# Performance work log

Measured on AMD Instinct MI355X. Metric: run time of the kernel, lower is better.

Reference implementation:

```python
import jax, jax.numpy as jnp
import numpy as np

B, N, F, U = 4, 4096, 256, 128
NEG = -1.0e9


def setup_inputs() -> dict:
    key = jax.random.key(0)
    k1, k2, k3, k4, k5 = jax.random.split(key, 5)
    inputs = jax.random.normal(k1, (B, N, F), dtype=jnp.float32)
    # Glorot-normal-like scales
    w = jax.random.normal(k2, (F, U), dtype=jnp.float32) * np.sqrt(2.0 / (F + U)).astype(np.float32)
    ai = jax.random.normal(k3, (U, N), dtype=jnp.float32) * np.sqrt(2.0 / (U + N)).astype(np.float32)
    aj = jax.random.normal(k4, (U, N), dtype=jnp.float32) * np.sqrt(2.0 / (U + N)).astype(np.float32)
    a = (jax.random.uniform(k5, (N, N)) < 0.004).astype(jnp.float32)
    adj = jnp.maximum(a, a.T)
    return {"inputs": inputs, "w": w, "ai": ai, "aj": aj, "adj": adj}


def reference(inputs, w, ai, aj, adj):
    # f: [B, N, U]
    f = jnp.einsum('bnf,fu->bnu', inputs, w)
    # self_attn[b,i,j] = (f ai)[b,i,j]; other_attn = transpose([0,2,1]) of (f aj)
    self_attn = jnp.einsum('bnu,um->bnm', f, ai)          # [B, N, N]
    other_attn = jnp.einsum('bnu,um->bmn', f, aj)         # transposed [B, N, N]
    mask = adj + jnp.eye(N, dtype=adj.dtype)              # allow self + neighbors
    attn = self_attn + other_attn + NEG * (1.0 - mask)
    attn = jax.nn.softmax(attn, axis=1)                   # softmax over rows (axis=1)
    # out[b,j,u] = sum_i f[b,i,u] * attn[b,i,j]
    out = jnp.einsum('biu,bij->bju', f, attn)
    return jax.nn.relu(out), attn
```

## Files before the change

kernel.cpp:

```cpp
#include <hip/hip_runtime.h>
#include <hip/hip_bf16.h>

#define NN 4096
#define UU 128
#define BB 4
#define FF 256
#define MAXD 128

__device__ __forceinline__ unsigned short f2bf(float x) {
    unsigned int u = __float_as_uint(x);
    unsigned int r = (u + 0x7fffu + ((u >> 16) & 1u)) >> 16;
    return (unsigned short)r;
}
__device__ __forceinline__ float bf2f(unsigned short h) {
    return __uint_as_float(((unsigned int)h) << 16);
}

template <int CTRL, int RMASK>
__device__ __forceinline__ float dpp_step(float x) {
    int ti = __builtin_amdgcn_update_dpp(0, __float_as_int(x), CTRL, RMASK, 0xf, true);
    return x + __int_as_float(ti);
}
__device__ __forceinline__ float wave_sum_dpp(float x) {
    x = dpp_step<0x111, 0xf>(x);
    x = dpp_step<0x112, 0xf>(x);
    x = dpp_step<0x114, 0xf>(x);
    x = dpp_step<0x118, 0xf>(x);
    x = dpp_step<0x142, 0xa>(x);
    x = dpp_step<0x143, 0xc>(x);
    return __int_as_float(__builtin_amdgcn_readlane(__float_as_int(x), 63));
}

__global__ __launch_bounds__(256) void transpose2(const float* __restrict__ ai,
                                                  const float* __restrict__ aj,
                                                  unsigned short* __restrict__ aiT,
                                                  unsigned short* __restrict__ ajT) {
    __shared__ float tile[32][33];
    const float* src = blockIdx.z ? aj : ai;
    unsigned short* dst = blockIdx.z ? ajT : aiT;
    int n0 = blockIdx.x * 32;
    int u0 = blockIdx.y * 32;
    int tx = threadIdx.x;
    int ty = threadIdx.y;
    for (int r = 0; r < 32; r += 8)
        tile[ty + r][tx] = src[(size_t)(u0 + ty + r) * NN + n0 + tx];
    __syncthreads();
    for (int r = 0; r < 32; r += 8)
        dst[(size_t)(n0 + ty + r) * UU + u0 + tx] = f2bf(tile[tx][ty + r]);
}

__global__ __launch_bounds__(256) void fgemm(const float* __restrict__ A,
                                             const float* __restrict__ Wm,
                                             unsigned short* __restrict__ F) {
    __shared__ float As[64][36];
    __shared__ float Ws[64][132];
    int t = threadIdx.x;
    int r0 = blockIdx.x * 32;
    int cg = t & 31;
    int rg = t >> 5;
    float acc[4][4] = {};

    for (int kc = 0; kc < FF; kc += 64) {
        {
            int row = t >> 3;
            int kb = (t & 7) * 8;
            const float* ap = A + (size_t)(r0 + row) * FF + kc + kb;
            float4 v0 = *(const float4*)(ap);
            float4 v1 = *(const float4*)(ap + 4);
            As[kb + 0][row] = v0.x; As[kb + 1][row] = v0.y;
            As[kb + 2][row] = v0.z; As[kb + 3][row] = v0.w;
            As[kb + 4][row] = v1.x; As[kb + 5][row] = v1.y;
            As[kb + 6][row] = v1.z; As[kb + 7][row] = v1.w;
        }
#pragma unroll
        for (int q = 0; q < 8; q++) {
            int idx = q * 256 + t;
            int k = idx >> 5;
            int c4 = (idx & 31) * 4;
            *(float4*)&Ws[k][c4] = *(const float4*)(Wm + (size_t)(kc + k) * UU + c4);
        }
        __syncthreads();
#pragma unroll 8
        for (int kk = 0; kk < 64; kk++) {
            float4 a4 = *(const float4*)&As[kk][rg * 4];
            float4 w4 = *(const float4*)&Ws[kk][cg * 4];
            acc[0][0] += a4.x * w4.x; acc[0][1] += a4.x * w4.y; acc[0][2] += a4.x * w4.z; acc[0][3] += a4.x * w4.w;
            acc[1][0] += a4.y * w4.x; acc[1][1] += a4.y * w4.y; acc[1][2] += a4.y * w4.z; acc[1][3] += a4.y * w4.w;
            acc[2][0] += a4.z * w4.x; acc[2][1] += a4.z * w4.y; acc[2][2] += a4.z * w4.z; acc[2][3] += a4.z * w4.w;
            acc[3][0] += a4.w * w4.x; acc[3][1] += a4.w * w4.y; acc[3][2] += a4.w * w4.z; acc[3][3] += a4.w * w4.w;
        }
        __syncthreads();
    }
#pragma unroll
    for (int i = 0; i < 4; i++) {
        ushort4 h;
        h.x = f2bf(acc[i][0]); h.y = f2bf(acc[i][1]);
        h.z = f2bf(acc[i][2]); h.w = f2bf(acc[i][3]);
        *(ushort4*)(F + (size_t)(r0 + rg * 4 + i) * UU + cg * 4) = h;
    }
}

__global__ __launch_bounds__(256) void scan_adj(const float* __restrict__ adj,
                                                unsigned short* __restrict__ csc,
                                                int* __restrict__ cnt,
                                                int* __restrict__ dblf) {
    __shared__ unsigned short tmp[MAXD];
    __shared__ int c, d;
    int j = blockIdx.x, tid = threadIdx.x;
    if (tid == 0) { c = 0; d = 0; }
    __syncthreads();
    const float4* row = (const float4*)(adj + (size_t)j * NN);
#pragma unroll
    for (int k = 0; k < 4; k++) {
        int q = tid + k * 256;
        float4 v = row[q];
        int base = q * 4;
        float vals[4] = {v.x, v.y, v.z, v.w};
#pragma unroll
        for (int t = 0; t < 4; t++) {
            int i = base + t;
            bool nz = (vals[t] != 0.0f);
            if (i == j) { if (nz) d = 1; nz = true; }
            if (nz) {
                int p = atomicAdd(&c, 1);
                if (p < MAXD) tmp[p] = (unsigned short)i;
            }
        }
    }
    __syncthreads();
    int M = c < MAXD ? c : MAXD;
    if (tid < M) csc[(size_t)j * MAXD + tid] = tmp[tid];
    if (tid == 0) { cnt[j] = M; dblf[j] = d; }
}

__global__ __launch_bounds__(256) void gat_cols(const unsigned short* __restrict__ csc,
                                                const int* __restrict__ cnt,
                                                const int* __restrict__ dblf,
                                                const unsigned short* __restrict__ f,
                                                const unsigned short* __restrict__ aiT,
                                                const unsigned short* __restrict__ ajT,
                                                float* __restrict__ out,
                                                float* __restrict__ attn) {
    __shared__ unsigned short sidx[MAXD];
    int j = blockIdx.x, tid = threadIdx.x;
    int lane = tid & 63, b = tid >> 6;
    int M = cnt[j];
    int oneh = dblf[j];
    if (tid < MAXD) sidx[tid] = csc[(size_t)j * MAXD + tid];

    const unsigned short* fb = f + (size_t)b * NN * UU;
    ushort2 fjh = *(const ushort2*)(fb + (size_t)j * UU + 2 * lane);
    float fjx = bf2f(fjh.x), fjy = bf2f(fjh.y);

    if (oneh) {
        if (lane == 0) attn[((size_t)(b * NN + j)) * NN + j] = 1.0f;
        float2 o;
        o.x = fjx > 0.0f ? fjx : 0.0f;
        o.y = fjy > 0.0f ? fjy : 0.0f;
        *(float2*)(out + ((size_t)(b * NN + j)) * UU + 2 * lane) = o;
        return;
    }
    __syncthreads();

    ushort2 aih = *(const ushort2*)(aiT + (size_t)j * UU + 2 * lane);
    float aix = bf2f(aih.x), aiy = bf2f(aih.y);
    float denom = 0.0f, acc0 = 0.0f, acc1 = 0.0f;
    float keep0 = 0.0f, keep1 = 0.0f;
    for (int e = 0; e < M; e++) {
        int i = sidx[e];
        ushort2 fih = *(const ushort2*)(fb + (size_t)i * UU + 2 * lane);
        ushort2 ajh = *(const ushort2*)(ajT + (size_t)i * UU + 2 * lane);
        float fix = bf2f(fih.x), fiy = bf2f(fih.y);
        float p = fix * aix + fiy * aiy + fjx * bf2f(ajh.x) + fjy * bf2f(ajh.y);
        float ex = __expf(wave_sum_dpp(p));
        denom += ex;
        acc0 += ex * fix;
        acc1 += ex * fiy;
        if ((e & 63) == lane) { if (e < 64) keep0 = ex; else keep1 = ex; }
    }
    float inv = 1.0f / denom;

    float2 o;
    o.x = acc0 * inv; o.y = acc1 * inv;
    o.x = o.x > 0.0f ? o.x : 0.0f;
    o.y = o.y > 0.0f ? o.y : 0.0f;
    *(float2*)(out + ((size_t)(b * NN + j)) * UU + 2 * lane) = o;

    if (lane < M)
        attn[((size_t)(b * NN + sidx[lane])) * NN + j] = keep0 * inv;
    if (lane + 64 < M)
        attn[((size_t)(b * NN + sidx[lane + 64])) * NN + j] = keep1 * inv;
}

extern "C" void kernel_launch(void* const* d_in, const int* in_sizes, int n_in,
                              void* d_out, int out_size, void* d_ws, size_t ws_size,
                              hipStream_t stream) {
    const float* inputs = (const float*)d_in[0];
    const float* w      = (const float*)d_in[1];
    const float* ai     = (const float*)d_in[2];
    const float* aj     = (const float*)d_in[3];
    const float* adj    = (const float*)d_in[4];

    float* out  = (float*)d_out;
    float* attn = out + (size_t)BB * NN * UU;

    unsigned short* f   = (unsigned short*)d_ws;
    unsigned short* aiT = f + (size_t)BB * NN * UU;
    unsigned short* ajT = aiT + (size_t)NN * UU;
    unsigned short* csc = ajT + (size_t)NN * UU;
    int* cnt  = (int*)(csc + (size_t)NN * MAXD);
    int* dblf = cnt + NN;

    (void)hipMemsetAsync(attn, 0, (size_t)BB * NN * NN * sizeof(float), stream);

    transpose2<<<dim3(NN / 32, UU / 32, 2), dim3(32, 8), 0, stream>>>(ai, aj, aiT, ajT);
    fgemm<<<dim3((BB * NN) / 32), 256, 0, stream>>>(inputs, w, f);
    scan_adj<<<NN, 256, 0, stream>>>(adj, csc, cnt, dblf);
    gat_cols<<<NN, 256, 0, stream>>>(csc, cnt, dblf, f, aiT, ajT, out, attn);
}
```

Measured before the change: 429.2 us.

## Fuse attn zero-fill into GAT kernel and defer sparse scatter to separate pass

Replaces the separate memset of the 256MB attention output with extra blocks in the GAT kernel that zero it using nontemporal vector stores. This lets zeroing overlap with the sparse attention compute. Softmax weights are staged to a workspace buffer, and a new kernel scatters them into attn after zeroing is guaranteed complete. The cost is one extra launch and a small staging buffer, and the gain depends on whether the fused zero blocks run faster than hipMemset.

```diff
diff --git a/kernel.cpp b/kernel.cpp
--- a/kernel.cpp
+++ b/kernel.cpp
@@ -6,6 +6,9 @@
 #define BB 4
 #define FF 256
 #define MAXD 128
+#define ZB 1024
+
+typedef float fv4 __attribute__((ext_vector_type(4)));
 
 __device__ __forceinline__ unsigned short f2bf(float x) {
     unsigned int u = __float_as_uint(x);
@@ -133,27 +136,43 @@
     if (tid == 0) { cnt[j] = M; dblf[j] = d; }
 }
 
-__global__ __launch_bounds__(256) void gat_cols(const unsigned short* __restrict__ csc,
-                                                const int* __restrict__ cnt,
-                                                const int* __restrict__ dblf,
-                                                const unsigned short* __restrict__ f,
-                                                const unsigned short* __restrict__ aiT,
-                                                const unsigned short* __restrict__ ajT,
-                                                float* __restrict__ out,
-                                                float* __restrict__ attn) {
+__global__ __launch_bounds__(256) void gat_zc(const unsigned short* __restrict__ csc,
+                                              const int* __restrict__ cnt,
+                                              const int* __restrict__ dblf,
+                                              const unsigned short* __restrict__ f,
+                                              const unsigned short* __restrict__ aiT,
+                                              const unsigned short* __restrict__ ajT,
+                                              float* __restrict__ out,
+                                              float* __restrict__ tmpex,
+                                              float* __restrict__ attn) {
+    int tid = threadIdx.x;
+    if (blockIdx.x >= NN) {
+        size_t base = (size_t)(blockIdx.x - NN) * ((size_t)BB * NN * NN / ZB);
+        fv4* p = (fv4*)(attn + base) + tid;
+        fv4 z = {0.f, 0.f, 0.f, 0.f};
+#pragma unroll 8
+        for (int q = 0; q < 64; q++)
+            __builtin_nontemporal_store(z, p + q * 256);
+        return;
+    }
+
     __shared__ unsigned short sidx[MAXD];
-    int j = blockIdx.x, tid = threadIdx.x;
+    int j = blockIdx.x;
     int lane = tid & 63, b = tid >> 6;
     int M = cnt[j];
     int oneh = dblf[j];
     if (tid < MAXD) sidx[tid] = csc[(size_t)j * MAXD + tid];
 
     const unsigned short* fb = f + (size_t)b * NN * UU;
+    float* te = tmpex + ((size_t)b * NN + j) * MAXD;
     ushort2 fjh = *(const ushort2*)(fb + (size_t)j * UU + 2 * lane);
     float fjx = bf2f(fjh.x), fjy = bf2f(fjh.y);
 
     if (oneh) {
-        if (lane == 0) attn[((size_t)(b * NN + j)) * NN + j] = 1.0f;
+        int g0 = csc[(size_t)j * MAXD + lane];
+        int g1 = csc[(size_t)j * MAXD + lane + 64];
+        if (lane < M)      te[lane]      = (g0 == j) ? 1.0f : 0.0f;
+        if (lane + 64 < M) te[lane + 64] = (g1 == j) ? 1.0f : 0.0f;
         float2 o;
         o.x = fjx > 0.0f ? fjx : 0.0f;
         o.y = fjy > 0.0f ? fjy : 0.0f;
@@ -186,10 +205,26 @@
     o.y = o.y > 0.0f ? o.y : 0.0f;
     *(float2*)(out + ((size_t)(b * NN + j)) * UU + 2 * lane) = o;
 
-    if (lane < M)
-        attn[((size_t)(b * NN + sidx[lane])) * NN + j] = keep0 * inv;
-    if (lane + 64 < M)
-        attn[((size_t)(b * NN + sidx[lane + 64])) * NN + j] = keep1 * inv;
+    if (lane < M)      te[lane]      = keep0 * inv;
+    if (lane + 64 < M) te[lane + 64] = keep1 * inv;
+}
+
+__global__ __launch_bounds__(256) void attn_scatter(const unsigned short* __restrict__ csc,
+                                                    const int* __restrict__ cnt,
+                                                    const float* __restrict__ tmpex,
+                                                    float* __restrict__ attn) {
+    int j = blockIdx.x, tid = threadIdx.x;
+    int lane = tid & 63, b = tid >> 6;
+    int M = cnt[j];
+    const float* te = tmpex + ((size_t)b * NN + j) * MAXD;
+    if (lane < M) {
+        int i = csc[(size_t)j * MAXD + lane];
+        __builtin_nontemporal_store(te[lane], &attn[((size_t)(b * NN + i)) * NN + j]);
+    }
+    if (lane + 64 < M) {
+        int i = csc[(size_t)j * MAXD + lane + 64];
+        __builtin_nontemporal_store(te[lane + 64], &attn[((size_t)(b * NN + i)) * NN + j]);
+    }
 }
 
 extern "C" void kernel_launch(void* const* d_in, const int* in_sizes, int n_in,
@@ -210,11 +245,11 @@
     unsigned short* csc = ajT + (size_t)NN * UU;
     int* cnt  = (int*)(csc + (size_t)NN * MAXD);
     int* dblf = cnt + NN;
-
-    (void)hipMemsetAsync(attn, 0, (size_t)BB * NN * NN * sizeof(float), stream);
+    float* tmpex = (float*)(dblf + NN);
 
     transpose2<<<dim3(NN / 32, UU / 32, 2), dim3(32, 8), 0, stream>>>(ai, aj, aiT, ajT);
     fgemm<<<dim3((BB * NN) / 32), 256, 0, stream>>>(inputs, w, f);
     scan_adj<<<NN, 256, 0, stream>>>(adj, csc, cnt, dblf);
-    gat_cols<<<NN, 256, 0, stream>>>(csc, cnt, dblf, f, aiT, ajT, out, attn);
-}
+    gat_zc<<<NN + ZB, 256, 0, stream>>>(csc, cnt, dblf, f, aiT, ajT, out, tmpex, attn);
+    attn_scatter<<<NN, 256, 0, stream>>>(csc, cnt, tmpex, attn);
+}
```

Result: faster. 419.2 us (-2.3%).
